# Kernel optimization log

Measured on AMD Instinct MI355X. Metric: run time of the kernel, lower is better.

Reference implementation:

```python
import jax, jax.numpy as jnp
import numpy as np

HIDDEN = 7168
NUM_EXPERTS = 256
TOPK = 8
NUM_GROUPS = 8
TOPK_GROUPS = 4
ROUTE_SCALE = 2.5
TOKENS = 8192


def setup_inputs() -> dict:
    key = jax.random.key(0)
    kx, kw = jax.random.split(key)
    x = jax.random.normal(kx, (TOKENS, HIDDEN), dtype=jnp.float32)
    # gate weight ~ nn.Parameter(empty) initialized here with small normal values
    weight = jax.random.normal(kw, (NUM_EXPERTS, HIDDEN), dtype=jnp.float32) * 0.02
    # bias branch is active because hidden_size == 7168
    bias = jnp.zeros((NUM_EXPERTS,), dtype=jnp.float32)
    return {"x": x, "weight": weight, "bias": bias}


def reference(x, weight, bias):
    # scores: [T, E] = sigmoid(x @ W^T)
    scores = jax.nn.sigmoid(jnp.einsum("th,eh->te", x.astype(jnp.float32), weight))
    original_scores = scores
    scores_for_choice = scores + bias  # bias is not None (hidden==7168)

    T = scores.shape[0]
    per_group = NUM_EXPERTS // NUM_GROUPS  # 32
    g = scores_for_choice.reshape(T, NUM_GROUPS, per_group)
    # bias is not None -> group score = sum of top-2 within each group
    group_scores = jax.lax.top_k(g, 2)[0].sum(axis=-1)  # [T, G]
    _, group_idx = jax.lax.top_k(group_scores, TOPK_GROUPS)  # [T, topk_groups]
    # keep-mask over groups
    keep = jnp.zeros((T, NUM_GROUPS), dtype=bool)
    keep = keep.at[jnp.arange(T)[:, None], group_idx].set(True)
    masked = jnp.where(keep[:, :, None], g, -jnp.inf).reshape(T, NUM_EXPERTS)

    _, indices = jax.lax.top_k(masked, TOPK)  # [T, topk]
    weights = jnp.take_along_axis(original_scores, indices, axis=1)
    weights = weights / (weights.sum(axis=-1, keepdims=True) + 1e-20)
    weights = weights * ROUTE_SCALE
    return weights.astype(jnp.float32), indices
```

## Files before the change

kernel.cpp:

```cpp
#include <hip/hip_runtime.h>
#include <math.h>


constexpr int T_TOK = 8192;
constexpr int HID   = 7168;
constexpr int NEXP  = 256;

constexpr int BM   = 64;
constexpr int BK   = 64;
constexpr int KSPL = 2;
constexpr int KH   = HID / KSPL;
constexpr int NIT  = KH / BK;

typedef __attribute__((ext_vector_type(8))) _Float16 hf8;
typedef __attribute__((ext_vector_type(4))) _Float16 hf4;
typedef __attribute__((ext_vector_type(4))) float    f32x4;

struct hl16 { _Float16 h, l; };
__device__ __forceinline__ hl16 cvt_split(float v, float scale) {
  const float s = v * scale;
  const _Float16 h = (_Float16)s;
  const _Float16 l = (_Float16)(s - (float)h);
  return {h, l};
}

__global__ __launch_bounds__(256)
void convert_w(const float* __restrict__ w, _Float16* __restrict__ wh,
               _Float16* __restrict__ wl) {
  const int gid = blockIdx.x * 256 + threadIdx.x;
  const int e = gid / (HID / 4);
  const int c = gid - e * (HID / 4);
  const float4 v = *(const float4*)(w + (size_t)gid * 4);
  const int k = 4 * c;
  const size_t o = (size_t)(k >> 3) * (NEXP * 8) + (size_t)e * 8 + (k & 7);
  hf4 h, l;
  hl16 t;
  t = cvt_split(v.x, 1024.f); h.x = t.h; l.x = t.l;
  t = cvt_split(v.y, 1024.f); h.y = t.h; l.y = t.l;
  t = cvt_split(v.z, 1024.f); h.z = t.h; l.z = t.l;
  t = cvt_split(v.w, 1024.f); h.w = t.h; l.w = t.l;
  *(hf4*)(wh + o) = h;
  *(hf4*)(wl + o) = l;
}

__global__ __launch_bounds__(512, 2)
void gemm_mfma(const float* __restrict__ x, const _Float16* __restrict__ wh,
               const _Float16* __restrict__ wl, float* __restrict__ part) {
  __shared__ __attribute__((aligned(16))) _Float16 Ah[2][BM * BK];
  __shared__ __attribute__((aligned(16))) _Float16 Al[2][BM * BK];

  const int tid = threadIdx.x;
  const int l   = tid & 63;
  const int wv  = tid >> 6;
  const int wm  = wv >> 2;
  const int wn  = wv & 3;
  const int kp  = blockIdx.x;
  const int t0  = blockIdx.y * BM;
  const int kb  = kp * KH;

  const int sr = tid >> 3;
  const int sc = tid & 7;
  const float* xrow = x + (size_t)(t0 + sr) * HID + kb + 4 * sc;

  const int swz   = (l & 7) << 4;
  const int rbyte = (wm * 32 + (l & 15)) * (BK * 2);
  const int kb16  = (l >> 4) * 16;

  const _Float16* bhb = wh + ((size_t)(kb >> 3) + (l >> 4)) * (NEXP * 8)
                           + (size_t)(wn * 64 + (l & 15)) * 8;
  const _Float16* blb = wl + ((size_t)(kb >> 3) + (l >> 4)) * (NEXP * 8)
                           + (size_t)(wn * 64 + (l & 15)) * 8;

  f32x4 acc[2][4] = {};

  float4 xv0 = *(const float4*)(xrow);
  float4 xv1 = *(const float4*)(xrow + 32);

#pragma unroll 2
  for (int it = 0; it < NIT; ++it) {
    hf8 bh[2][4], bl[2][4];
    const _Float16* bhi = bhb + (size_t)it * (8 * NEXP * 8);
    const _Float16* bli = blb + (size_t)it * (8 * NEXP * 8);
#pragma unroll
    for (int s = 0; s < 2; ++s)
#pragma unroll
      for (int nf = 0; nf < 4; ++nf) {
        bh[s][nf] = *(const hf8*)(bhi + s * (4 * NEXP * 8) + nf * 128);
        bl[s][nf] = *(const hf8*)(bli + s * (4 * NEXP * 8) + nf * 128);
      }

    _Float16* ah = &Ah[it & 1][0];
    _Float16* al = &Al[it & 1][0];
    {
      hf4 h0, h1, g0, g1;
      hl16 t;
      t = cvt_split(xv0.x, 64.f); h0.x = t.h; g0.x = t.l;
      t = cvt_split(xv0.y, 64.f); h0.y = t.h; g0.y = t.l;
      t = cvt_split(xv0.z, 64.f); h0.z = t.h; g0.z = t.l;
      t = cvt_split(xv0.w, 64.f); h0.w = t.h; g0.w = t.l;
      t = cvt_split(xv1.x, 64.f); h1.x = t.h; g1.x = t.l;
      t = cvt_split(xv1.y, 64.f); h1.y = t.h; g1.y = t.l;
      t = cvt_split(xv1.z, 64.f); h1.z = t.h; g1.z = t.l;
      t = cvt_split(xv1.w, 64.f); h1.w = t.h; g1.w = t.l;
      const int wb = sr * (BK * 2);
      const int wsw = (sr & 7) << 4;
      *(hf4*)((char*)ah + wb + ((sc * 8)      ^ wsw)) = h0;
      *(hf4*)((char*)ah + wb + ((sc * 8 + 64) ^ wsw)) = h1;
      *(hf4*)((char*)al + wb + ((sc * 8)      ^ wsw)) = g0;
      *(hf4*)((char*)al + wb + ((sc * 8 + 64) ^ wsw)) = g1;
    }

    if (it + 1 < NIT) {
      xv0 = *(const float4*)(xrow + (it + 1) * BK);
      xv1 = *(const float4*)(xrow + (it + 1) * BK + 32);
    }

    asm volatile("s_waitcnt lgkmcnt(0)\n\ts_barrier" ::: "memory");

#pragma unroll
    for (int s = 0; s < 2; ++s) {
      hf8 af[2], afl[2];
#pragma unroll
      for (int mf = 0; mf < 2; ++mf) {
        const int off = rbyte + mf * (16 * BK * 2) + ((kb16 + s * 64) ^ swz);
        af[mf]  = *(const hf8*)((const char*)ah + off);
        afl[mf] = *(const hf8*)((const char*)al + off);
      }
#pragma unroll
      for (int mf = 0; mf < 2; ++mf)
#pragma unroll
        for (int nf = 0; nf < 4; ++nf) {
          acc[mf][nf] = __builtin_amdgcn_mfma_f32_16x16x32_f16(
              af[mf],  bh[s][nf], acc[mf][nf], 0, 0, 0);
          acc[mf][nf] = __builtin_amdgcn_mfma_f32_16x16x32_f16(
              afl[mf], bh[s][nf], acc[mf][nf], 0, 0, 0);
          acc[mf][nf] = __builtin_amdgcn_mfma_f32_16x16x32_f16(
              af[mf],  bl[s][nf], acc[mf][nf], 0, 0, 0);
        }
    }
  }

  float* pout = part + (size_t)kp * ((size_t)T_TOK * NEXP);
  const int eb = wn * 64 + (l & 15);
  const int tb = t0 + wm * 32 + ((l >> 4) << 2);
#pragma unroll
  for (int mf = 0; mf < 2; ++mf)
#pragma unroll
    for (int j = 0; j < 4; ++j) {
      float* pr = pout + (size_t)(tb + mf * 16 + j) * NEXP + eb;
#pragma unroll
      for (int nf = 0; nf < 4; ++nf) pr[nf * 16] = acc[mf][nf][j];
    }
}

__global__ __launch_bounds__(256)
void routing_kernel(const float* __restrict__ part,
                    const float* __restrict__ bias,
                    float* __restrict__ out) {
  const int lane = threadIdx.x & 63;
  const int t = blockIdx.x * 4 + (threadIdx.x >> 6);
  const int e_base = 4 * lane;

  float4 z = make_float4(0.f, 0.f, 0.f, 0.f);
#pragma unroll
  for (int kp = 0; kp < KSPL; ++kp) {
    float4 v = *(const float4*)(part + (size_t)kp * T_TOK * NEXP +
                                (size_t)t * NEXP + e_base);
    z.x += v.x; z.y += v.y; z.z += v.z; z.w += v.w;
  }
  constexpr float INV = 1.f / 65536.f;
  float s[4], sb[4];
  const float4 b4 = *(const float4*)(bias + e_base);
  s[0] = 1.f / (1.f + expf(-z.x * INV)); sb[0] = s[0] + b4.x;
  s[1] = 1.f / (1.f + expf(-z.y * INV)); sb[1] = s[1] + b4.y;
  s[2] = 1.f / (1.f + expf(-z.z * INV)); sb[2] = s[2] + b4.z;
  s[3] = 1.f / (1.f + expf(-z.w * INV)); sb[3] = s[3] + b4.w;

  const float Ma = fmaxf(sb[0], sb[1]), ma = fminf(sb[0], sb[1]);
  const float Mb = fmaxf(sb[2], sb[3]), mb = fminf(sb[2], sb[3]);
  float m1 = fmaxf(Ma, Mb);
  float m2 = fmaxf(fminf(Ma, Mb), fmaxf(ma, mb));
#pragma unroll
  for (int off = 1; off < 8; off <<= 1) {
    const float o1 = __shfl_xor(m1, off);
    const float o2 = __shfl_xor(m2, off);
    const float n1 = fmaxf(m1, o1);
    m2 = fmaxf(fminf(m1, o1), fmaxf(m2, o2));
    m1 = n1;
  }
  const float gsum = m1 + m2;

  float gs[8];
#pragma unroll
  for (int g = 0; g < 8; ++g) gs[g] = __shfl(gsum, g * 8);

  unsigned gmask = 0;
#pragma unroll
  for (int r = 0; r < 4; ++r) {
    int best = 0; float bv = -3.4e38f;
#pragma unroll
    for (int g = 0; g < 8; ++g) {
      const bool ok = (((gmask >> g) & 1u) == 0) && (gs[g] > bv);
      bv = ok ? gs[g] : bv;
      best = ok ? g : best;
    }
    gmask |= 1u << best;
  }

  const bool sel = (gmask >> (lane >> 3)) & 1u;
#pragma unroll
  for (int j = 0; j < 4; ++j) sb[j] = sel ? sb[j] : -3.4e38f;

  float wq[8]; float iq[8];
#pragma unroll
  for (int r = 0; r < 8; ++r) {
    float bv = sb[0]; int bi = e_base; float bs = s[0];
#pragma unroll
    for (int j = 1; j < 4; ++j) {
      const bool c = sb[j] > bv;
      bv = c ? sb[j] : bv; bi = c ? e_base + j : bi; bs = c ? s[j] : bs;
    }
#pragma unroll
    for (int off = 1; off < 64; off <<= 1) {
      const float ov = __shfl_xor(bv, off);
      const int   oi = __shfl_xor(bi, off);
      const float os = __shfl_xor(bs, off);
      const bool take = (ov > bv) || (ov == bv && oi < bi);
      bv = take ? ov : bv; bi = take ? oi : bi; bs = take ? os : bs;
    }
    wq[r] = bs; iq[r] = (float)bi;
#pragma unroll
    for (int j = 0; j < 4; ++j)
      if (e_base + j == bi) sb[j] = -3.4e38f;
  }

  float wsum = 1e-20f;
#pragma unroll
  for (int r = 0; r < 8; ++r) wsum += wq[r];
  const float scale = 2.5f / wsum;

  if (lane == 0) {
    float4* ow = (float4*)(out + (size_t)t * 8);
    ow[0] = make_float4(wq[0] * scale, wq[1] * scale, wq[2] * scale, wq[3] * scale);
    ow[1] = make_float4(wq[4] * scale, wq[5] * scale, wq[6] * scale, wq[7] * scale);
    float4* oi = (float4*)(out + (size_t)T_TOK * 8 + (size_t)t * 8);
    oi[0] = make_float4(iq[0], iq[1], iq[2], iq[3]);
    oi[1] = make_float4(iq[4], iq[5], iq[6], iq[7]);
  }
}

extern "C" void kernel_launch(void* const* d_in, const int* in_sizes, int n_in,
                              void* d_out, int out_size, void* d_ws, size_t ws_size,
                              hipStream_t stream) {
  const float* x    = (const float*)d_in[0];
  const float* w    = (const float*)d_in[1];
  const float* bias = (const float*)d_in[2];
  float* out  = (float*)d_out;
  float* part = (float*)d_ws;
  _Float16* wh = (_Float16*)((char*)d_ws + (size_t)KSPL * T_TOK * NEXP * 4);
  _Float16* wl = wh + (size_t)NEXP * HID;

  hipLaunchKernelGGL(convert_w, dim3(NEXP * HID / 4 / 256), dim3(256), 0,
                     stream, w, wh, wl);
  hipLaunchKernelGGL(gemm_mfma, dim3(KSPL, T_TOK / BM), dim3(512), 0, stream,
                     x, wh, wl, part);
  hipLaunchKernelGGL(routing_kernel, dim3(T_TOK / 4), dim3(256), 0, stream,
                     part, bias, out);
}
```

Baseline: 396.7 us.

## Switch GEMM to 32x32x16 MFMA tiles with 4-way K split and block remap

Each wave now covers a 64x32 output tile with two 32x32x16 MFMA accumulators instead of a grid of 16x16x32 fragments. The K dimension is split four ways, giving 512 blocks on a remapped 1D grid, and launch bounds now target four blocks per CU. The next x tile is prefetched at the top of each iteration so the global load overlaps the MFMA work. The aim is more parallelism and fewer MFMA instructions for the same tile. The cost is twice the partial-sum traffic into the routing kernel and more register pressure under the higher occupancy target.

```diff
diff --git a/kernel.cpp b/kernel.cpp
--- a/kernel.cpp
+++ b/kernel.cpp
@@ -8,13 +8,13 @@
 
 constexpr int BM   = 64;
 constexpr int BK   = 64;
-constexpr int KSPL = 2;
+constexpr int KSPL = 4;
 constexpr int KH   = HID / KSPL;
 constexpr int NIT  = KH / BK;
 
-typedef __attribute__((ext_vector_type(8))) _Float16 hf8;
-typedef __attribute__((ext_vector_type(4))) _Float16 hf4;
-typedef __attribute__((ext_vector_type(4))) float    f32x4;
+typedef __attribute__((ext_vector_type(8)))  _Float16 hf8;
+typedef __attribute__((ext_vector_type(4)))  _Float16 hf4;
+typedef __attribute__((ext_vector_type(16))) float    f32x16;
 
 struct hl16 { _Float16 h, l; };
 __device__ __forceinline__ hl16 cvt_split(float v, float scale) {
@@ -43,7 +43,7 @@
   *(hf4*)(wl + o) = l;
 }
 
-__global__ __launch_bounds__(512, 2)
+__global__ __launch_bounds__(512, 4)
 void gemm_mfma(const float* __restrict__ x, const _Float16* __restrict__ wh,
                const _Float16* __restrict__ wl, float* __restrict__ part) {
   __shared__ __attribute__((aligned(16))) _Float16 Ah[2][BM * BK];
@@ -51,43 +51,49 @@
 
   const int tid = threadIdx.x;
   const int l   = tid & 63;
-  const int wv  = tid >> 6;
-  const int wm  = wv >> 2;
-  const int wn  = wv & 3;
-  const int kp  = blockIdx.x;
-  const int t0  = blockIdx.y * BM;
-  const int kb  = kp * KH;
+  const int wn  = tid >> 6;
+
+  const int b  = blockIdx.x;
+  const int kp = (b & 7) >> 1;
+  const int tt = (b >> 3) + 64 * (b & 1);
+  const int t0 = tt * BM;
+  const int kb = kp * KH;
 
   const int sr = tid >> 3;
   const int sc = tid & 7;
   const float* xrow = x + (size_t)(t0 + sr) * HID + kb + 4 * sc;
 
   const int swz   = (l & 7) << 4;
-  const int rbyte = (wm * 32 + (l & 15)) * (BK * 2);
-  const int kb16  = (l >> 4) * 16;
-
-  const _Float16* bhb = wh + ((size_t)(kb >> 3) + (l >> 4)) * (NEXP * 8)
-                           + (size_t)(wn * 64 + (l & 15)) * 8;
-  const _Float16* blb = wl + ((size_t)(kb >> 3) + (l >> 4)) * (NEXP * 8)
-                           + (size_t)(wn * 64 + (l & 15)) * 8;
-
-  f32x4 acc[2][4] = {};
+  const int lrow  = l & 31;
+  const int khalf = l >> 5;
+
+  const _Float16* bhb = wh + ((size_t)(kb >> 3) + khalf) * (NEXP * 8)
+                           + (size_t)(wn * 32 + lrow) * 8;
+  const _Float16* blb = wl + ((size_t)(kb >> 3) + khalf) * (NEXP * 8)
+                           + (size_t)(wn * 32 + lrow) * 8;
+
+  f32x16 acc[2] = {};
 
   float4 xv0 = *(const float4*)(xrow);
   float4 xv1 = *(const float4*)(xrow + 32);
 
 #pragma unroll 2
   for (int it = 0; it < NIT; ++it) {
-    hf8 bh[2][4], bl[2][4];
+    float4 xn0, xn1;
+    const bool more = (it + 1 < NIT);
+    if (more) {
+      xn0 = *(const float4*)(xrow + (it + 1) * BK);
+      xn1 = *(const float4*)(xrow + (it + 1) * BK + 32);
+    }
+
+    hf8 bh[4], bl[4];
     const _Float16* bhi = bhb + (size_t)it * (8 * NEXP * 8);
     const _Float16* bli = blb + (size_t)it * (8 * NEXP * 8);
 #pragma unroll
-    for (int s = 0; s < 2; ++s)
-#pragma unroll
-      for (int nf = 0; nf < 4; ++nf) {
-        bh[s][nf] = *(const hf8*)(bhi + s * (4 * NEXP * 8) + nf * 128);
-        bl[s][nf] = *(const hf8*)(bli + s * (4 * NEXP * 8) + nf * 128);
-      }
+    for (int ks = 0; ks < 4; ++ks) {
+      bh[ks] = *(const hf8*)(bhi + ks * (2 * NEXP * 8));
+      bl[ks] = *(const hf8*)(bli + ks * (2 * NEXP * 8));
+    }
 
     _Float16* ah = &Ah[it & 1][0];
     _Float16* al = &Al[it & 1][0];
@@ -102,7 +108,7 @@
       t = cvt_split(xv1.y, 64.f); h1.y = t.h; g1.y = t.l;
       t = cvt_split(xv1.z, 64.f); h1.z = t.h; g1.z = t.l;
       t = cvt_split(xv1.w, 64.f); h1.w = t.h; g1.w = t.l;
-      const int wb = sr * (BK * 2);
+      const int wb  = sr * (BK * 2);
       const int wsw = (sr & 7) << 4;
       *(hf4*)((char*)ah + wb + ((sc * 8)      ^ wsw)) = h0;
       *(hf4*)((char*)ah + wb + ((sc * 8 + 64) ^ wsw)) = h1;
@@ -110,46 +116,36 @@
       *(hf4*)((char*)al + wb + ((sc * 8 + 64) ^ wsw)) = g1;
     }
 
-    if (it + 1 < NIT) {
-      xv0 = *(const float4*)(xrow + (it + 1) * BK);
-      xv1 = *(const float4*)(xrow + (it + 1) * BK + 32);
-    }
-
     asm volatile("s_waitcnt lgkmcnt(0)\n\ts_barrier" ::: "memory");
 
 #pragma unroll
-    for (int s = 0; s < 2; ++s) {
-      hf8 af[2], afl[2];
-#pragma unroll
-      for (int mf = 0; mf < 2; ++mf) {
-        const int off = rbyte + mf * (16 * BK * 2) + ((kb16 + s * 64) ^ swz);
-        af[mf]  = *(const hf8*)((const char*)ah + off);
-        afl[mf] = *(const hf8*)((const char*)al + off);
-      }
-#pragma unroll
-      for (int mf = 0; mf < 2; ++mf)
-#pragma unroll
-        for (int nf = 0; nf < 4; ++nf) {
-          acc[mf][nf] = __builtin_amdgcn_mfma_f32_16x16x32_f16(
-              af[mf],  bh[s][nf], acc[mf][nf], 0, 0, 0);
-          acc[mf][nf] = __builtin_amdgcn_mfma_f32_16x16x32_f16(
-              afl[mf], bh[s][nf], acc[mf][nf], 0, 0, 0);
-          acc[mf][nf] = __builtin_amdgcn_mfma_f32_16x16x32_f16(
-              af[mf],  bl[s][nf], acc[mf][nf], 0, 0, 0);
-        }
-    }
+    for (int ks = 0; ks < 4; ++ks) {
+      const int cb = (ks * 32 + khalf * 16) ^ swz;
+      const hf8 a0h = *(const hf8*)((const char*)ah + lrow * 128 + cb);
+      const hf8 a1h = *(const hf8*)((const char*)ah + (32 + lrow) * 128 + cb);
+      const hf8 a0l = *(const hf8*)((const char*)al + lrow * 128 + cb);
+      const hf8 a1l = *(const hf8*)((const char*)al + (32 + lrow) * 128 + cb);
+      acc[0] = __builtin_amdgcn_mfma_f32_32x32x16_f16(a0h, bh[ks], acc[0], 0, 0, 0);
+      acc[1] = __builtin_amdgcn_mfma_f32_32x32x16_f16(a1h, bh[ks], acc[1], 0, 0, 0);
+      acc[0] = __builtin_amdgcn_mfma_f32_32x32x16_f16(a0l, bh[ks], acc[0], 0, 0, 0);
+      acc[1] = __builtin_amdgcn_mfma_f32_32x32x16_f16(a1l, bh[ks], acc[1], 0, 0, 0);
+      acc[0] = __builtin_amdgcn_mfma_f32_32x32x16_f16(a0h, bl[ks], acc[0], 0, 0, 0);
+      acc[1] = __builtin_amdgcn_mfma_f32_32x32x16_f16(a1h, bl[ks], acc[1], 0, 0, 0);
+    }
+
+    if (more) { xv0 = xn0; xv1 = xn1; }
   }
 
   float* pout = part + (size_t)kp * ((size_t)T_TOK * NEXP);
-  const int eb = wn * 64 + (l & 15);
-  const int tb = t0 + wm * 32 + ((l >> 4) << 2);
-#pragma unroll
-  for (int mf = 0; mf < 2; ++mf)
-#pragma unroll
-    for (int j = 0; j < 4; ++j) {
-      float* pr = pout + (size_t)(tb + mf * 16 + j) * NEXP + eb;
-#pragma unroll
-      for (int nf = 0; nf < 4; ++nf) pr[nf * 16] = acc[mf][nf][j];
+  const int e = wn * 32 + lrow;
+#pragma unroll
+  for (int mt = 0; mt < 2; ++mt)
+#pragma unroll
+    for (int g = 0; g < 4; ++g) {
+      const int r0 = t0 + mt * 32 + 8 * g + 4 * khalf;
+#pragma unroll
+      for (int j = 0; j < 4; ++j)
+        pout[(size_t)(r0 + j) * NEXP + e] = acc[mt][4 * g + j];
     }
 }
 
@@ -262,7 +258,7 @@
 
   hipLaunchKernelGGL(convert_w, dim3(NEXP * HID / 4 / 256), dim3(256), 0,
                      stream, w, wh, wl);
-  hipLaunchKernelGGL(gemm_mfma, dim3(KSPL, T_TOK / BM), dim3(512), 0, stream,
+  hipLaunchKernelGGL(gemm_mfma, dim3(512), dim3(512), 0, stream,
                      x, wh, wl, part);
   hipLaunchKernelGGL(routing_kernel, dim3(T_TOK / 4), dim3(256), 0, stream,
                      part, bias, out);
```

Result: faster. 383.9 us (-3.2%).
